# Kernel optimization log

Measured on AMD Instinct MI355X. Metric: run time of the kernel, lower is better.

The kernel has to match this reference:

```python
import jax, jax.numpy as jnp
import numpy as np

B, T, H = 2, 2048, 1024
DFF = 4 * H        # dense_mlp hidden width
E = 8              # num_experts_temp
TOP_K = 2


def setup_inputs() -> dict:
    key = jax.random.key(0)
    ks = jax.random.split(key, 6)
    s_h = 1.0 / np.sqrt(H)
    s_f = 1.0 / np.sqrt(DFF)
    return {
        "hidden_states": jax.random.normal(ks[0], (B, T, H), dtype=jnp.float32),
        "router_w": jax.random.normal(ks[1], (E, H), dtype=jnp.float32) * s_h,
        "w1": jax.random.normal(ks[2], (E, H, DFF), dtype=jnp.float32) * s_h,
        "b1": jnp.zeros((E, DFF), dtype=jnp.float32),
        "w2": jax.random.normal(ks[3], (E, DFF, H), dtype=jnp.float32) * s_f,
        "b2": jnp.zeros((E, H), dtype=jnp.float32),
    }


def reference(hidden_states, router_w, w1, b1, w2, b2):
    # Router: [B,T,E]
    router_logits = jnp.einsum("bth,eh->bte", hidden_states, router_w)
    topk_vals, topk_idx = jax.lax.top_k(router_logits, TOP_K)        # [B,T,K]
    topk_w = jax.nn.softmax(topk_vals.astype(jnp.float32), axis=-1)
    topk_w = topk_w.astype(hidden_states.dtype)

    # Dense compute of ALL experts (faithful to the original module).
    h = jnp.einsum("bth,ehf->btef", hidden_states, w1) + b1          # [B,T,E,DFF]
    h = jax.nn.gelu(h)
    expert_out = jnp.einsum("btef,efh->bteh", h, w2) + b2            # [B,T,E,H]

    # Gather top-k experts per token and mix.
    topk_out = jnp.take_along_axis(expert_out, topk_idx[..., None], axis=2)  # [B,T,K,H]
    mixed = jnp.sum(topk_out * topk_w[..., None], axis=2)            # [B,T,H]
    return mixed
```

## Files before the change

### kernel.cpp

```cpp
#include <hip/hip_runtime.h>
#include <hip/hip_bf16.h>
#include <stdint.h>

#define AS1 __attribute__((address_space(1)))
#define AS3 __attribute__((address_space(3)))

typedef __bf16 bf16x8 __attribute__((ext_vector_type(8)));
typedef float floatx4 __attribute__((ext_vector_type(4)));

static constexpr int NTOK = 4096;
static constexpr int H    = 1024;
static constexpr int DFF  = 4096;
static constexpr int E    = 8;
static constexpr int BM   = 128;
static constexpr int BN   = 128;
static constexpr int MAXROWS = 9216;

static constexpr size_t OFF_WS    = 0;
static constexpr size_t OFF_XCS   = 67108864;
static constexpr size_t OFF_HS    = 85983232;
static constexpr size_t OFF_RTIDX = 161480704;
static constexpr size_t OFF_RTW   = 161513472;
static constexpr size_t OFF_PTOK  = 161546240;
static constexpr size_t OFF_PW    = 161583104;
static constexpr size_t OFF_CNT   = 161619968;
static constexpr size_t WS_NEED   = 161620068;

__device__ __forceinline__ unsigned short f2bf(float f) {
    __bf16 b = (__bf16)f;
    return __builtin_bit_cast(unsigned short, b);
}

__device__ __forceinline__ void gload16(const void* g, void* l) {
    __builtin_amdgcn_global_load_lds((AS1 void*)g, (AS3 void*)l, 16, 0, 0);
}

__global__ __launch_bounds__(256) void k_router(const float* __restrict__ x,
                                                const float* __restrict__ rw,
                                                int* __restrict__ rt_idx,
                                                float* __restrict__ rt_w,
                                                int* __restrict__ counts) {
    const int wv = threadIdx.x >> 6, ln = threadIdx.x & 63;
    const int t = blockIdx.x * 4 + wv;
    const float* xr = x + (size_t)t * H + ln * 4;
    float4 xv[4];
#pragma unroll
    for (int c = 0; c < 4; ++c) xv[c] = *(const float4*)(xr + c * 256);
    float lg[E];
#pragma unroll
    for (int e = 0; e < E; ++e) {
        const float* rr = rw + (size_t)e * H + ln * 4;
        float acc = 0.f;
#pragma unroll
        for (int c = 0; c < 4; ++c) {
            float4 rv = *(const float4*)(rr + c * 256);
            acc += xv[c].x * rv.x + xv[c].y * rv.y + xv[c].z * rv.z + xv[c].w * rv.w;
        }
#pragma unroll
        for (int s = 32; s > 0; s >>= 1) acc += __shfl_xor(acc, s, 64);
        lg[e] = acc;
    }
    if (ln == 0) {
        int i0 = 0; float v0 = lg[0];
#pragma unroll
        for (int e = 1; e < E; ++e) if (lg[e] > v0) { v0 = lg[e]; i0 = e; }
        int i1 = -1; float v1 = -INFINITY;
#pragma unroll
        for (int e = 0; e < E; ++e) if (e != i0 && lg[e] > v1) { v1 = lg[e]; i1 = e; }
        float e1 = expf(v1 - v0);
        float inv = 1.f / (1.f + e1);
        rt_idx[2 * t] = i0; rt_idx[2 * t + 1] = i1;
        rt_w[2 * t] = inv;  rt_w[2 * t + 1] = e1 * inv;
        atomicAdd(&counts[i0], 1);
        atomicAdd(&counts[i1], 1);
    }
}

__global__ void k_offsets(const int* __restrict__ counts, int* __restrict__ offs) {
    if (threadIdx.x == 0) {
        int o = 0;
        for (int e = 0; e < E; ++e) { offs[e] = o; o += (counts[e] + BM - 1) & ~(BM - 1); }
        offs[E] = o;
    }
}

__global__ __launch_bounds__(256) void k_scatter(const int* __restrict__ rt_idx,
                                                 const float* __restrict__ rt_w,
                                                 const int* __restrict__ offs,
                                                 int* __restrict__ cursors,
                                                 int* __restrict__ pair_tok,
                                                 float* __restrict__ pair_w) {
    int t = blockIdx.x * 256 + threadIdx.x;
    if (t >= NTOK) return;
    for (int k = 0; k < 2; ++k) {
        int e = rt_idx[2 * t + k];
        int p = atomicAdd(&cursors[e], 1);
        int pos = offs[e] + p;
        pair_tok[pos] = t;
        pair_w[pos] = rt_w[2 * t + k];
    }
}

__global__ __launch_bounds__(256) void k_gather(const float* __restrict__ x,
                                                const int* __restrict__ offs,
                                                const int* __restrict__ counts,
                                                const int* __restrict__ pair_tok,
                                                unsigned short* __restrict__ xcs) {
    int pos = blockIdx.x;
    if (pos >= offs[E]) return;
    int e = 0;
    while (e < E - 1 && pos >= offs[e + 1]) ++e;
    bool valid = (pos - offs[e]) < counts[e];
    int tok = valid ? pair_tok[pos] : 0;
    int k0 = threadIdx.x * 4;
    float4 xv = valid ? *(const float4*)(x + (size_t)tok * H + k0)
                      : make_float4(0.f, 0.f, 0.f, 0.f);
    ushort4 o;
    o.x = f2bf(xv.x); o.y = f2bf(xv.y); o.z = f2bf(xv.z); o.w = f2bf(xv.w);
    int rb = pos >> 7, m = pos & 127;
    size_t idx = (((size_t)(rb * 32 + (k0 >> 5)) * 128 + m) * 32) + (((k0 >> 3) & 3) << 3) + (k0 & 7);
    *(ushort4*)(xcs + idx) = o;
}

template <int K, int N>
__global__ __launch_bounds__(256) void k_convert(const float* __restrict__ w,
                                                 unsigned short* __restrict__ ws) {
    constexpr int KB = K / 32, NB = N / 64;
    int bid = blockIdx.x;
    int nb = bid % NB, kb = (bid / NB) % KB, e = bid / (NB * KB);
    int kq = threadIdx.x & 3, nl = threadIdx.x >> 2;
    int n = nb * 64 + nl;
    const float* src = w + ((size_t)e * K + kb * 32 + kq * 8) * N + n;
    union { unsigned short us[8]; uint4 v; } u;
#pragma unroll
    for (int j = 0; j < 8; ++j) u.us[j] = f2bf(src[(size_t)j * N]);
    size_t oct = ((size_t)(e * KB + kb) * N + n) * 4 + kq;
    *(uint4*)(ws + oct * 8) = u.v;
}

template <int KTOT, int NTOT, bool IS_GEMM1>
__global__ __launch_bounds__(256) void k_gemm(const unsigned short* __restrict__ Asrc,
                                              const unsigned short* __restrict__ Bsrc,
                                              const int* __restrict__ counts,
                                              const int* __restrict__ offs,
                                              const float* __restrict__ bias,
                                              const int* __restrict__ pair_tok,
                                              const float* __restrict__ pair_w,
                                              unsigned short* __restrict__ Hs,
                                              float* __restrict__ out) {
    constexpr int KB = KTOT / 32;
    const int e = blockIdx.y >> 5, rt = blockIdx.y & 31;
    const int cnt = counts[e];
    if (rt * BM >= cnt) return;
    const int off = offs[e];
    const int rb = (off >> 7) + rt;
    const int n0 = blockIdx.x * BN;

    __shared__ unsigned short lds_a[BM * 32];
    __shared__ unsigned short lds_b[BN * 32];

    const int tid = threadIdx.x;
    const int wv = tid >> 6, ln = tid & 63;
    const int quad = ln >> 4, lr = ln & 15;
    const int wm = (wv & 1) * 64, wn = (wv >> 1) * 64;

    floatx4 acc[4][4];
#pragma unroll
    for (int i = 0; i < 4; ++i)
#pragma unroll
        for (int j = 0; j < 4; ++j) acc[i][j] = (floatx4){0.f, 0.f, 0.f, 0.f};

    const unsigned short* Atile = Asrc + (size_t)rb * KB * 4096;
    const unsigned short* Btile = Bsrc + ((size_t)e * KB * NTOT + n0) * 32;

    for (int kb = 0; kb < KB; ++kb) {
        __syncthreads();
        const unsigned short* a_src = Atile + (size_t)kb * 4096 + (wv * 2) * 512 + ln * 8;
        const unsigned short* b_src = Btile + (size_t)kb * NTOT * 32 + (wv * 2) * 512 + ln * 8;
#pragma unroll
        for (int c = 0; c < 2; ++c) {
            gload16(a_src + c * 512, &lds_a[(wv * 2 + c) * 512]);
            gload16(b_src + c * 512, &lds_b[(wv * 2 + c) * 512]);
        }
        __syncthreads();
        bf16x8 af[4], bg[4];
#pragma unroll
        for (int i = 0; i < 4; ++i) {
            af[i] = *(const bf16x8*)(lds_a + (wm + i * 16 + lr) * 32 + quad * 8);
            bg[i] = *(const bf16x8*)(lds_b + (wn + i * 16 + lr) * 32 + quad * 8);
        }
#pragma unroll
        for (int i = 0; i < 4; ++i)
#pragma unroll
            for (int j = 0; j < 4; ++j)
                acc[i][j] = __builtin_amdgcn_mfma_f32_16x16x32_bf16(af[i], bg[j], acc[i][j], 0, 0, 0);
    }

    if (IS_GEMM1) {
        float bj[4];
#pragma unroll
        for (int j = 0; j < 4; ++j) bj[j] = bias[(size_t)e * NTOT + n0 + wn + j * 16 + lr];
#pragma unroll
        for (int i = 0; i < 4; ++i) {
#pragma unroll
            for (int j = 0; j < 4; ++j) {
                const int f = n0 + wn + j * 16 + lr;
                const size_t fbase = (((size_t)rb * 128 + (f >> 5)) * 128) * 32 + (((f >> 3) & 3) << 3) + (f & 7);
#pragma unroll
                for (int r = 0; r < 4; ++r) {
                    const int m = wm + i * 16 + quad * 4 + r;
                    float v = acc[i][j][r] + bj[j];
                    float u = v + 0.044715f * v * v * v;
                    float tz = tanhf(0.79788456080286535588f * u);
                    float g = 0.5f * v * (1.f + tz);
                    Hs[fbase + (size_t)m * 32] = f2bf(g);
                }
            }
        }
    } else {
        float bj[4];
#pragma unroll
        for (int j = 0; j < 4; ++j) bj[j] = bias[(size_t)e * NTOT + n0 + wn + j * 16 + lr];
#pragma unroll
        for (int i = 0; i < 4; ++i) {
#pragma unroll
            for (int r = 0; r < 4; ++r) {
                const int m = wm + i * 16 + quad * 4 + r;
                const int lm = rt * BM + m;
                if (lm < cnt) {
                    const int pos = off + lm;
                    const int tok = pair_tok[pos];
                    const float wgt = pair_w[pos];
#pragma unroll
                    for (int j = 0; j < 4; ++j) {
                        const int n = n0 + wn + j * 16 + lr;
                        unsafeAtomicAdd(&out[(size_t)tok * H + n], wgt * (acc[i][j][r] + bj[j]));
                    }
                }
            }
        }
    }
}

extern "C" void kernel_launch(void* const* d_in, const int* in_sizes, int n_in,
                              void* d_out, int out_size, void* d_ws, size_t ws_size,
                              hipStream_t stream) {
    const float* x  = (const float*)d_in[0];
    const float* rw = (const float*)d_in[1];
    const float* w1 = (const float*)d_in[2];
    const float* b1 = (const float*)d_in[3];
    const float* w2 = (const float*)d_in[4];
    const float* b2 = (const float*)d_in[5];
    float* out = (float*)d_out;
    char* ws = (char*)d_ws;
    if (ws_size < WS_NEED) return;

    unsigned short* Ws   = (unsigned short*)(ws + OFF_WS);
    unsigned short* XcS  = (unsigned short*)(ws + OFF_XCS);
    unsigned short* Hs   = (unsigned short*)(ws + OFF_HS);
    int*   rt_idx   = (int*)(ws + OFF_RTIDX);
    float* rt_w     = (float*)(ws + OFF_RTW);
    int*   pair_tok = (int*)(ws + OFF_PTOK);
    float* pair_w   = (float*)(ws + OFF_PW);
    int*   cnt      = (int*)(ws + OFF_CNT);
    int*   cur      = cnt + 8;
    int*   offs     = cnt + 16;

    hipMemsetAsync(cnt, 0, 64, stream);
    hipMemsetAsync(out, 0, (size_t)out_size * 4, stream);

    k_router<<<NTOK / 4, 256, 0, stream>>>(x, rw, rt_idx, rt_w, cnt);
    k_offsets<<<1, 64, 0, stream>>>(cnt, offs);
    k_scatter<<<NTOK / 256, 256, 0, stream>>>(rt_idx, rt_w, offs, cur, pair_tok, pair_w);
    k_gather<<<MAXROWS, 256, 0, stream>>>(x, offs, cnt, pair_tok, XcS);

    k_convert<H, DFF><<<8 * (H / 32) * (DFF / 64), 256, 0, stream>>>(w1, Ws);
    k_gemm<H, DFF, true><<<dim3(DFF / BN, 256), 256, 0, stream>>>(
        XcS, Ws, cnt, offs, b1, pair_tok, pair_w, Hs, out);

    k_convert<DFF, H><<<8 * (DFF / 32) * (H / 64), 256, 0, stream>>>(w2, Ws);
    k_gemm<DFF, H, false><<<dim3(H / BN, 256), 256, 0, stream>>>(
        Hs, Ws, cnt, offs, b2, pair_tok, pair_w, Hs, out);
}
```

Measured before the change: 711.1 us.

## Split-K second GEMM, stage GEMM1 epilogue through LDS, use exp-based GELU

The second expert GEMM is split four ways along K through a z grid dimension. Partial sums are combined through the existing atomic adds, and the bias is applied only by the first split. This adds blocks to a launch that previously had few active tiles. The first GEMM's epilogue now writes GELU results into padded LDS and then stores them to global memory with coalesced 16-byte writes, replacing scattered 2-byte stores. It also computes tanh-GELU through __expf instead of tanhf. The cost is four times as many atomics in GEMM2, and some extra synchronisation and LDS use in GEMM1.

```diff
diff --git a/kernel.cpp b/kernel.cpp
--- a/kernel.cpp
+++ b/kernel.cpp
@@ -138,7 +138,7 @@
     *(uint4*)(ws + oct * 8) = u.v;
 }
 
-template <int KTOT, int NTOT, bool IS_GEMM1>
+template <int KTOT, int NTOT, bool IS_GEMM1, int KSPLIT>
 __global__ __launch_bounds__(256) void k_gemm(const unsigned short* __restrict__ Asrc,
                                               const unsigned short* __restrict__ Bsrc,
                                               const int* __restrict__ counts,
@@ -148,16 +148,22 @@
                                               const float* __restrict__ pair_w,
                                               unsigned short* __restrict__ Hs,
                                               float* __restrict__ out) {
-    constexpr int KB = KTOT / 32;
+    constexpr int KB  = KTOT / 32;
+    constexpr int KBS = KB / KSPLIT;
+    constexpr int MP  = 36;
+    constexpr int SMEM_SHORTS = IS_GEMM1 ? (4 * 128 * MP) : 8192;
+
     const int e = blockIdx.y >> 5, rt = blockIdx.y & 31;
     const int cnt = counts[e];
     if (rt * BM >= cnt) return;
+    const int ks = blockIdx.z;
     const int off = offs[e];
     const int rb = (off >> 7) + rt;
     const int n0 = blockIdx.x * BN;
 
-    __shared__ unsigned short lds_a[BM * 32];
-    __shared__ unsigned short lds_b[BN * 32];
+    __shared__ unsigned short smem[SMEM_SHORTS];
+    unsigned short* lds_a = smem;
+    unsigned short* lds_b = smem + 4096;
 
     const int tid = threadIdx.x;
     const int wv = tid >> 6, ln = tid & 63;
@@ -173,7 +179,7 @@
     const unsigned short* Atile = Asrc + (size_t)rb * KB * 4096;
     const unsigned short* Btile = Bsrc + ((size_t)e * KB * NTOT + n0) * 32;
 
-    for (int kb = 0; kb < KB; ++kb) {
+    for (int kb = ks * KBS; kb < ks * KBS + KBS; ++kb) {
         __syncthreads();
         const unsigned short* a_src = Atile + (size_t)kb * 4096 + (wv * 2) * 512 + ln * 8;
         const unsigned short* b_src = Btile + (size_t)kb * NTOT * 32 + (wv * 2) * 512 + ln * 8;
@@ -200,27 +206,42 @@
         float bj[4];
 #pragma unroll
         for (int j = 0; j < 4; ++j) bj[j] = bias[(size_t)e * NTOT + n0 + wn + j * 16 + lr];
-#pragma unroll
-        for (int i = 0; i < 4; ++i) {
-#pragma unroll
-            for (int j = 0; j < 4; ++j) {
-                const int f = n0 + wn + j * 16 + lr;
-                const size_t fbase = (((size_t)rb * 128 + (f >> 5)) * 128) * 32 + (((f >> 3) & 3) << 3) + (f & 7);
+        __syncthreads();
+#pragma unroll
+        for (int j = 0; j < 4; ++j) {
+            const int fl = wn + j * 16 + lr;
+            const int fb = fl >> 5, f5 = fl & 31;
+            unsigned short* dst = smem + fb * (128 * MP) + f5;
+#pragma unroll
+            for (int i = 0; i < 4; ++i) {
 #pragma unroll
                 for (int r = 0; r < 4; ++r) {
                     const int m = wm + i * 16 + quad * 4 + r;
                     float v = acc[i][j][r] + bj[j];
-                    float u = v + 0.044715f * v * v * v;
-                    float tz = tanhf(0.79788456080286535588f * u);
-                    float g = 0.5f * v * (1.f + tz);
-                    Hs[fbase + (size_t)m * 32] = f2bf(g);
+                    float u = 0.79788456080286535588f * (v + 0.044715f * v * v * v);
+                    float ez = __expf(2.f * u);
+                    float g = v * (1.f - 1.f / (ez + 1.f));
+                    dst[m * MP] = f2bf(g);
                 }
             }
         }
+        __syncthreads();
+        const size_t hsbase = ((size_t)rb * 128 + (n0 >> 5)) * 4096;
+#pragma unroll
+        for (int it = 0; it < 8; ++it) {
+            const int g = (it * 256 + tid) * 8;
+            const int fb = g >> 12, rem = g & 4095, m = rem >> 5, f5 = rem & 31;
+            const unsigned short* s = smem + fb * (128 * MP) + m * MP + f5;
+            uint2 lo = *(const uint2*)s;
+            uint2 hi = *(const uint2*)(s + 4);
+            uint4 v4 = make_uint4(lo.x, lo.y, hi.x, hi.y);
+            *(uint4*)(Hs + hsbase + (size_t)g) = v4;
+        }
     } else {
         float bj[4];
 #pragma unroll
-        for (int j = 0; j < 4; ++j) bj[j] = bias[(size_t)e * NTOT + n0 + wn + j * 16 + lr];
+        for (int j = 0; j < 4; ++j)
+            bj[j] = (ks == 0) ? bias[(size_t)e * NTOT + n0 + wn + j * 16 + lr] : 0.f;
 #pragma unroll
         for (int i = 0; i < 4; ++i) {
 #pragma unroll
@@ -275,10 +296,10 @@
     k_gather<<<MAXROWS, 256, 0, stream>>>(x, offs, cnt, pair_tok, XcS);
 
     k_convert<H, DFF><<<8 * (H / 32) * (DFF / 64), 256, 0, stream>>>(w1, Ws);
-    k_gemm<H, DFF, true><<<dim3(DFF / BN, 256), 256, 0, stream>>>(
+    k_gemm<H, DFF, true, 1><<<dim3(DFF / BN, 256, 1), 256, 0, stream>>>(
         XcS, Ws, cnt, offs, b1, pair_tok, pair_w, Hs, out);
 
     k_convert<DFF, H><<<8 * (DFF / 32) * (H / 64), 256, 0, stream>>>(w2, Ws);
-    k_gemm<DFF, H, false><<<dim3(H / BN, 256), 256, 0, stream>>>(
+    k_gemm<DFF, H, false, 4><<<dim3(H / BN, 256, 4), 256, 0, stream>>>(
         Hs, Ws, cnt, offs, b2, pair_tok, pair_w, Hs, out);
 }
```

New measurement: 738.3 us. +3.8%, slower.
